# Optimization experiments

Hardware: AMD Instinct MI355X
Metric: run time of the kernel (lower is better)

Reference implementation:

```python
import jax, jax.numpy as jnp
import numpy as np

SCALE = 4

def setup_inputs() -> dict:
    key = jax.random.key(0)
    # LR image batch in [0,1], as produced by torchvision ToTensor
    x = jax.random.uniform(key, (16, 3, 256, 256), dtype=jnp.float32)
    return {"x": x}

def reference(x) -> jnp.ndarray:
    if SCALE == 1:
        return x
    B, C, H, W = x.shape
    # PIL BICUBIC == Keys cubic kernel with a=-0.5; jax.image 'cubic' uses the
    # same kernel. Upscaling, so no antialias filtering differences apply.
    out_shape = (B, C, H * SCALE, W * SCALE)
    return jax.image.resize(x, out_shape, method="cubic")
```

## Files before the change

kernel.cpp:

```cpp
#include <hip/hip_runtime.h>


#define Hin 256
#define Win 256

__global__ __launch_bounds__(256) void cubic_up4(const float* __restrict__ in,
                                                 float* __restrict__ out) {
    const int jx = threadIdx.x;
    const int blk = blockIdx.x;
    const int jy = blk & (Hin - 1);
    const int bc = blk >> 8;

    const float* __restrict__ inp = in + (size_t)bc * (Hin * Win);
    float* __restrict__ outp = out + (size_t)bc * ((size_t)Hin * Win * 16);

    __shared__ float sv[5][Win];
#pragma unroll
    for (int r = 0; r < 5; ++r) {
        int ry = jy - 2 + r;
        ry = ry < 0 ? 0 : (ry > Hin - 1 ? Hin - 1 : ry);
        sv[r][jx] = inp[ry * Win + jx];
    }
    __syncthreads();

    const float WKc[4][4] = {
        {-0.0439453125f, 0.3896484375f, 0.7275390625f, -0.0732421875f},
        {-0.0068359375f, 0.0908203125f, 0.9638671875f, -0.0478515625f},
        {-0.0478515625f, 0.9638671875f, 0.0908203125f, -0.0068359375f},
        {-0.0732421875f, 0.7275390625f, 0.3896484375f, -0.0439453125f}};

    float wx[4][4];
#pragma unroll
    for (int r = 0; r < 4; ++r) {
        float s = 0.f;
#pragma unroll
        for (int t = 0; t < 4; ++t) {
            int c = jx - 2 + (r >> 1) + t;
            float w = (c >= 0 && c < Win) ? WKc[r][t] : 0.f;
            wx[r][t] = w;
            s += w;
        }
        float inv = 1.f / s;
#pragma unroll
        for (int t = 0; t < 4; ++t) wx[r][t] *= inv;
    }
    float wy[4][4];
#pragma unroll
    for (int r = 0; r < 4; ++r) {
        float s = 0.f;
#pragma unroll
        for (int t = 0; t < 4; ++t) {
            int c = jy - 2 + (r >> 1) + t;
            float w = (c >= 0 && c < Hin) ? WKc[r][t] : 0.f;
            wy[r][t] = w;
            s += w;
        }
        float inv = 1.f / s;
#pragma unroll
        for (int t = 0; t < 4; ++t) wy[r][t] *= inv;
    }

    float v[5][5];
#pragma unroll
    for (int k = 0; k < 5; ++k) {
        int c = jx - 2 + k;
        c = c < 0 ? 0 : (c > Win - 1 ? Win - 1 : c);
#pragma unroll
        for (int r = 0; r < 5; ++r) v[r][k] = sv[r][c];
    }

    float h[5][4];
#pragma unroll
    for (int r = 0; r < 5; ++r) {
#pragma unroll
        for (int rx = 0; rx < 4; ++rx) {
            int o = rx >> 1;
            h[r][rx] = wx[rx][0] * v[r][o] + wx[rx][1] * v[r][o + 1] +
                       wx[rx][2] * v[r][o + 2] + wx[rx][3] * v[r][o + 3];
        }
    }

#pragma unroll
    for (int ry = 0; ry < 4; ++ry) {
        int o = ry >> 1;
        float4 res;
        float* rp = (float*)&res;
#pragma unroll
        for (int rx = 0; rx < 4; ++rx) {
            rp[rx] = wy[ry][0] * h[o][rx] + wy[ry][1] * h[o + 1][rx] +
                     wy[ry][2] * h[o + 2][rx] + wy[ry][3] * h[o + 3][rx];
        }
        float4* dst = (float4*)(outp + (size_t)(4 * jy + ry) * (Win * 4) + 4 * jx);
        *dst = res;
    }
}

extern "C" void kernel_launch(void* const* d_in, const int* in_sizes, int n_in,
                              void* d_out, int out_size, void* d_ws, size_t ws_size,
                              hipStream_t stream) {
    const float* x = (const float*)d_in[0];
    float* out = (float*)d_out;
    cubic_up4<<<dim3(16 * 3 * 256), dim3(256), 0, stream>>>(x, out);
}
```

Before: 202.7 us.

## Process four input rows per block and specialize interior paths with constant weights

Each block now handles four input rows, loading an 8-row halo tile into padded shared memory instead of 5 rows per single input row. Interior threads use compile-time constant cubic weights, while edge threads and edge row-blocks keep the renormalized-weight path using fast reciprocal. This reduces redundant global/shared loads and per-thread weight arithmetic, at the cost of more registers and branch divergence at edges.

```diff
diff --git a/kernel.cpp b/kernel.cpp
--- a/kernel.cpp
+++ b/kernel.cpp
@@ -4,94 +4,140 @@
 #define Hin 256
 #define Win 256
 
-__global__ __launch_bounds__(256) void cubic_up4(const float* __restrict__ in,
-                                                 float* __restrict__ out) {
+#define WK00 -0.0439453125f
+#define WK01  0.3896484375f
+#define WK02  0.7275390625f
+#define WK03 -0.0732421875f
+#define WK10 -0.0068359375f
+#define WK11  0.0908203125f
+#define WK12  0.9638671875f
+#define WK13 -0.0478515625f
+
+__global__ __launch_bounds__(256, 4) void cubic_up4(const float* __restrict__ in,
+                                                    float* __restrict__ out) {
     const int jx = threadIdx.x;
-    const int blk = blockIdx.x;
-    const int jy = blk & (Hin - 1);
-    const int bc = blk >> 8;
+    const int jy4 = blockIdx.x & 63;
+    const int bc = blockIdx.x >> 6;
+    const int jy0 = jy4 << 2;
 
     const float* __restrict__ inp = in + (size_t)bc * (Hin * Win);
     float* __restrict__ outp = out + (size_t)bc * ((size_t)Hin * Win * 16);
 
-    __shared__ float sv[5][Win];
+    const float WK[4][4] = {{WK00, WK01, WK02, WK03},
+                            {WK10, WK11, WK12, WK13},
+                            {WK13, WK12, WK11, WK10},
+                            {WK03, WK02, WK01, WK00}};
+
+    __shared__ float sv[8][Win + 4];
 #pragma unroll
-    for (int r = 0; r < 5; ++r) {
-        int ry = jy - 2 + r;
+    for (int r = 0; r < 8; ++r) {
+        int ry = jy0 - 2 + r;
         ry = ry < 0 ? 0 : (ry > Hin - 1 ? Hin - 1 : ry);
-        sv[r][jx] = inp[ry * Win + jx];
+        sv[r][jx + 2] = inp[ry * Win + jx];
+    }
+    if (jx < 2) {
+#pragma unroll
+        for (int r = 0; r < 8; ++r) sv[r][jx] = 0.f;
+    }
+    if (jx >= Win - 2) {
+#pragma unroll
+        for (int r = 0; r < 8; ++r) sv[r][jx + 4] = 0.f;
     }
     __syncthreads();
 
-    const float WKc[4][4] = {
-        {-0.0439453125f, 0.3896484375f, 0.7275390625f, -0.0732421875f},
-        {-0.0068359375f, 0.0908203125f, 0.9638671875f, -0.0478515625f},
-        {-0.0478515625f, 0.9638671875f, 0.0908203125f, -0.0068359375f},
-        {-0.0732421875f, 0.7275390625f, 0.3896484375f, -0.0439453125f}};
-
-    float wx[4][4];
+    float h[8][4];
+    const bool xedge = (jx < 2) | (jx >= Win - 2);
+    if (!xedge) {
 #pragma unroll
-    for (int r = 0; r < 4; ++r) {
-        float s = 0.f;
+        for (int r = 0; r < 8; ++r) {
+            const float* p = &sv[r][jx];
+            const float a0 = p[0], a1 = p[1], a2 = p[2], a3 = p[3], a4 = p[4];
+            h[r][0] = WK00 * a0 + WK01 * a1 + WK02 * a2 + WK03 * a3;
+            h[r][1] = WK10 * a0 + WK11 * a1 + WK12 * a2 + WK13 * a3;
+            h[r][2] = WK13 * a1 + WK12 * a2 + WK11 * a3 + WK10 * a4;
+            h[r][3] = WK03 * a1 + WK02 * a2 + WK01 * a3 + WK00 * a4;
+        }
+    } else {
+        float wx[4][4];
 #pragma unroll
-        for (int t = 0; t < 4; ++t) {
-            int c = jx - 2 + (r >> 1) + t;
-            float w = (c >= 0 && c < Win) ? WKc[r][t] : 0.f;
-            wx[r][t] = w;
-            s += w;
+        for (int r = 0; r < 4; ++r) {
+            const int o = r >> 1;
+            float s = 0.f;
+#pragma unroll
+            for (int t = 0; t < 4; ++t) {
+                const int c = jx - 2 + o + t;
+                const float w = (c >= 0 && c < Win) ? WK[r][t] : 0.f;
+                wx[r][t] = w;
+                s += w;
+            }
+            const float inv = __builtin_amdgcn_rcpf(s);
+#pragma unroll
+            for (int t = 0; t < 4; ++t) wx[r][t] *= inv;
         }
-        float inv = 1.f / s;
 #pragma unroll
-        for (int t = 0; t < 4; ++t) wx[r][t] *= inv;
-    }
-    float wy[4][4];
+        for (int r = 0; r < 8; ++r) {
+            const float* p = &sv[r][jx];
 #pragma unroll
-    for (int r = 0; r < 4; ++r) {
-        float s = 0.f;
-#pragma unroll
-        for (int t = 0; t < 4; ++t) {
-            int c = jy - 2 + (r >> 1) + t;
-            float w = (c >= 0 && c < Hin) ? WKc[r][t] : 0.f;
-            wy[r][t] = w;
-            s += w;
-        }
-        float inv = 1.f / s;
-#pragma unroll
-        for (int t = 0; t < 4; ++t) wy[r][t] *= inv;
-    }
-
-    float v[5][5];
-#pragma unroll
-    for (int k = 0; k < 5; ++k) {
-        int c = jx - 2 + k;
-        c = c < 0 ? 0 : (c > Win - 1 ? Win - 1 : c);
-#pragma unroll
-        for (int r = 0; r < 5; ++r) v[r][k] = sv[r][c];
-    }
-
-    float h[5][4];
-#pragma unroll
-    for (int r = 0; r < 5; ++r) {
-#pragma unroll
-        for (int rx = 0; rx < 4; ++rx) {
-            int o = rx >> 1;
-            h[r][rx] = wx[rx][0] * v[r][o] + wx[rx][1] * v[r][o + 1] +
-                       wx[rx][2] * v[r][o + 2] + wx[rx][3] * v[r][o + 3];
+            for (int rx = 0; rx < 4; ++rx) {
+                const int o = rx >> 1;
+                h[r][rx] = wx[rx][0] * p[o] + wx[rx][1] * p[o + 1] +
+                           wx[rx][2] * p[o + 2] + wx[rx][3] * p[o + 3];
+            }
         }
     }
 
+    const bool yedge = (jy4 == 0) | (jy4 == 63);
+    if (!yedge) {
 #pragma unroll
-    for (int ry = 0; ry < 4; ++ry) {
-        int o = ry >> 1;
-        float4 res;
-        float* rp = (float*)&res;
+        for (int ty = 0; ty < 4; ++ty) {
 #pragma unroll
-        for (int rx = 0; rx < 4; ++rx) {
-            rp[rx] = wy[ry][0] * h[o][rx] + wy[ry][1] * h[o + 1][rx] +
-                     wy[ry][2] * h[o + 2][rx] + wy[ry][3] * h[o + 3][rx];
+            for (int ry = 0; ry < 4; ++ry) {
+                const int o = ty + (ry >> 1);
+                float4 res;
+                float* rp = (float*)&res;
+#pragma unroll
+                for (int rx = 0; rx < 4; ++rx) {
+                    rp[rx] = WK[ry][0] * h[o][rx] + WK[ry][1] * h[o + 1][rx] +
+                             WK[ry][2] * h[o + 2][rx] + WK[ry][3] * h[o + 3][rx];
+                }
+                *(float4*)(outp + (size_t)((jy4 << 4) + (ty << 2) + ry) * (Win * 4) +
+                           (jx << 2)) = res;
+            }
         }
-        float4* dst = (float4*)(outp + (size_t)(4 * jy + ry) * (Win * 4) + 4 * jx);
-        *dst = res;
+    } else {
+#pragma unroll
+        for (int ty = 0; ty < 4; ++ty) {
+            const int jy = jy0 + ty;
+            float wy[4][4];
+#pragma unroll
+            for (int r = 0; r < 4; ++r) {
+                const int o = r >> 1;
+                float s = 0.f;
+#pragma unroll
+                for (int t = 0; t < 4; ++t) {
+                    const int c = jy - 2 + o + t;
+                    const float w = (c >= 0 && c < Hin) ? WK[r][t] : 0.f;
+                    wy[r][t] = w;
+                    s += w;
+                }
+                const float inv = __builtin_amdgcn_rcpf(s);
+#pragma unroll
+                for (int t = 0; t < 4; ++t) wy[r][t] *= inv;
+            }
+#pragma unroll
+            for (int ry = 0; ry < 4; ++ry) {
+                const int o = ty + (ry >> 1);
+                float4 res;
+                float* rp = (float*)&res;
+#pragma unroll
+                for (int rx = 0; rx < 4; ++rx) {
+                    rp[rx] = wy[ry][0] * h[o][rx] + wy[ry][1] * h[o + 1][rx] +
+                             wy[ry][2] * h[o + 2][rx] + wy[ry][3] * h[o + 3][rx];
+                }
+                *(float4*)(outp + (size_t)((jy4 << 4) + (ty << 2) + ry) * (Win * 4) +
+                           (jx << 2)) = res;
+            }
+        }
     }
 }
 
@@ -100,5 +146,5 @@
                               hipStream_t stream) {
     const float* x = (const float*)d_in[0];
     float* out = (float*)d_out;
-    cubic_up4<<<dim3(16 * 3 * 256), dim3(256), 0, stream>>>(x, out);
+    cubic_up4<<<dim3(48 * 64), dim3(256), 0, stream>>>(x, out);
 }
```

Measured after the change: 199.9 us. About the same (-1.4%).
